# Kernel tuning notes

Hardware: AMD Instinct MI355X
Metric: run time of the kernel (lower is better)

Reference implementation:

```python
import jax, jax.numpy as jnp
import numpy as np

# ---- hardcoded module constants (from Cyborg.__init__) ----
B, S, V = 256, 128, 512
H = 30              # number of symbol vectors
N_STACKS = 2
R = 2               # REDUNDANCY
DEPTH = 4           # stack_depth
ZERO_OFFSET = 1e-6
NAND_BIAS = 3.0
INIT_SHARPEN = 10.0
N_VECS = 1 + N_STACKS  # input vec + one peek per stack = 3
C_BIG = (H + N_STACKS) * R   # 64 choices for push_fn / calc_out
C_SMALL = 2 * R              # 4 choices for pop_op / push_op


def _cossim(a, b, eps=1e-8):
    # torch.cosine_similarity semantics: per-vector norm clamp
    na = jnp.maximum(jnp.linalg.norm(a, axis=-1, keepdims=True), eps)
    nb = jnp.maximum(jnp.linalg.norm(b, axis=-1, keepdims=True), eps)
    return jnp.sum((a / na) * (b / nb), axis=-1)


def _nand(query, w, nw_raw):
    # Fuzzy-NAND gate bank (neurallambda NAND, clip='abs').
    # query: [B, N_VECS*V], w: [C, N_VECS*V], nw_raw: [C, N_VECS] -> [B, C]
    C = w.shape[0]
    q = query.reshape(-1, 1, N_VECS, V)
    wv = w.reshape(1, C, N_VECS, V)
    cos = jnp.abs(_cossim(q, wv))                 # [B, C, N_VECS], clip='abs'
    nw = jax.nn.sigmoid(nw_raw)[None]             # interpolate sim vs NOT(sim)
    interp = nw * cos + (1.0 - nw) * (1.0 - cos)
    return jnp.prod(interp, axis=-1)              # fuzzy AND over the 3 vecs


# ---- differentiable stack (soft pointer over DEPTH slots) ----
def _read(stack, ptr):
    return jnp.einsum('bdv,bd->bv', stack, ptr)

def _push(stack, ptr, val):
    p = jnp.roll(ptr, 1, axis=1)
    s = stack * (1.0 - p)[..., None] + val[:, None, :] * p[..., None]
    return s, p

def _pop(stack, ptr):
    s = stack * (1.0 - ptr)[..., None] + ZERO_OFFSET * ptr[..., None]
    p = jnp.roll(ptr, -1, axis=1)
    return s, p

def _pop_or_nop(stack, ptr, sharp, should_pop, should_nop):
    pr = jax.nn.softmax(jnp.stack([should_pop, should_nop], -1) * sharp, axis=-1)
    ps, pp = _pop(stack, ptr)
    s = ps * pr[:, 0, None, None] + stack * pr[:, 1, None, None]
    p = pp * pr[:, 0, None] + ptr * pr[:, 1, None]
    return s, p

def _push_or_nop(stack, ptr, sharp, should_push, should_nop, val):
    pr = jax.nn.softmax(jnp.stack([should_push, should_nop], -1) * sharp, axis=-1)
    ps, pp = _push(stack, ptr, val)
    s = ps * pr[:, 0, None, None] + stack * pr[:, 1, None, None]
    p = pp * pr[:, 0, None] + ptr * pr[:, 1, None]
    return s, p


def _forward(x, syms, stack_init_vec, sharp, pop_w, pop_nw, pushop_w, pushop_nw,
             pushfn_w, pushfn_nw, calc_w, calc_nw):
    b = x.shape[0]
    # init both stacks to zero_offset, pointer at slot 0, then hard-push init vec
    stack0 = jnp.full((N_STACKS, b, DEPTH, V), ZERO_OFFSET, x.dtype)
    ptr0 = jnp.zeros((N_STACKS, b, DEPTH), x.dtype).at[:, :, 0].set(1.0)
    init_val = jnp.broadcast_to(stack_init_vec, (b, V))
    stack0, ptr0 = jax.vmap(_push, in_axes=(0, 0, None))(stack0, ptr0, init_val)

    syms_b = jnp.broadcast_to(syms, (b, H, V))

    def step(carry, inp):
        stacks, ptrs = carry                                    # [2,B,D,V], [2,B,D]
        peeks = jax.vmap(_read)(stacks, ptrs)                   # [2,B,V]
        inps = jnp.concatenate([inp, peeks[0], peeks[1]], -1)   # [B,3V]
        out_opts = jnp.concatenate(
            [syms_b, peeks[0][:, None], peeks[1][:, None]], 1)  # [B,H+2,V]
        new_s, new_p = [], []
        for k in range(N_STACKS):
            pops = _nand(inps, pop_w[k], pop_nw[k])             # [B, 2R]
            pushes = _nand(inps, pushop_w[k], pushop_nw[k])     # [B, 2R]
            pv = _nand(inps, pushfn_w[k], pushfn_nw[k]).reshape(b, H + N_STACKS, R)
            push_val = jnp.einsum('bcv,bcr->bv', out_opts, pv)
            s, p = _pop_or_nop(stacks[k], ptrs[k], sharp[k],
                               pops[:, :R].max(1), pops[:, R:].max(1))
            s, p = _push_or_nop(s, p, sharp[k],
                                pushes[:, :R].max(1), pushes[:, R:].max(1), push_val)
            new_s.append(s)
            new_p.append(p)
        stacks = jnp.stack(new_s)
        ptrs = jnp.stack(new_p)
        peeks2 = jax.vmap(_read)(stacks, ptrs)
        inps2 = jnp.concatenate([inp, peeks2[0], peeks2[1]], -1)
        out_opts2 = jnp.concatenate(
            [syms_b, peeks2[0][:, None], peeks2[1][:, None]], 1)
        cv = _nand(inps2, calc_w, calc_nw).reshape(b, H + N_STACKS, R)
        out = jnp.einsum('bcv,bcr->bv', out_opts2, cv)
        return (stacks, ptrs), out

    _, outs = jax.lax.scan(step, (stack0, ptr0), jnp.swapaxes(x, 0, 1))
    return jnp.swapaxes(outs, 0, 1)  # [B,S,V]


def setup_inputs() -> dict:
    key = jax.random.key(0)
    ks = jax.random.split(key, 12)
    siv = jax.random.normal(ks[1], (V,), jnp.float32)
    siv = siv / jnp.linalg.norm(siv)
    return {
        'x': jax.random.normal(ks[0], (B, S, V), jnp.float32),
        'syms': jax.random.normal(ks[2], (H, V), jnp.float32),
        'stack_init_vec': siv,
        'sharp': jnp.full((N_STACKS,), INIT_SHARPEN, jnp.float32),
        'pop_w': jax.random.normal(ks[3], (N_STACKS, C_SMALL, N_VECS * V), jnp.float32),
        'pop_nw': jax.random.normal(ks[4], (N_STACKS, C_SMALL, N_VECS), jnp.float32) + NAND_BIAS,
        'pushop_w': jax.random.normal(ks[5], (N_STACKS, C_SMALL, N_VECS * V), jnp.float32),
        'pushop_nw': jax.random.normal(ks[6], (N_STACKS, C_SMALL, N_VECS), jnp.float32) + NAND_BIAS,
        'pushfn_w': jax.random.normal(ks[7], (N_STACKS, C_BIG, N_VECS * V), jnp.float32),
        'pushfn_nw': jax.random.normal(ks[8], (N_STACKS, C_BIG, N_VECS), jnp.float32) + NAND_BIAS,
        'calc_w': jax.random.normal(ks[9], (C_BIG, N_VECS * V), jnp.float32),
        'calc_nw': jax.random.normal(ks[10], (C_BIG, N_VECS), jnp.float32) + NAND_BIAS,
    }


def reference(x, syms, stack_init_vec, sharp, pop_w, pop_nw, pushop_w, pushop_nw,
              pushfn_w, pushfn_nw, calc_w, calc_nw):
    return _forward(x, syms, stack_init_vec, sharp, pop_w, pop_nw, pushop_w,
                    pushop_nw, pushfn_w, pushfn_nw, calc_w, calc_nw)
```

## Files before the change

### kernel.cpp

```cpp
#include <hip/hip_runtime.h>
#include <math.h>


#define SS 128
#define VV 512
#define NROWS 208
#define ZOFF 1e-6f

#define OFF_I0   0
#define OFF_OC   (32768*208)
#define OFF_GI   (OFF_OC + 32768*32)
#define OFF_M    (OFF_GI + 2*32*208)
#define OFF_A    (OFF_M + 1024)
#define OFF_Bc   (OFF_A + 624)
#define OFF_W0   (OFF_Bc + 624)

typedef _Float16 half8 __attribute__((ext_vector_type(8)));
typedef float f32x4 __attribute__((ext_vector_type(4)));
typedef float f32x2 __attribute__((ext_vector_type(2)));

__device__ __forceinline__ float rlane(float v, int lane) {
    return __int_as_float(__builtin_amdgcn_readlane(__float_as_int(v), lane));
}
template <int CTRL>
__device__ __forceinline__ float dpp_add(float x) {
    int y = __builtin_amdgcn_update_dpp(0, __float_as_int(x), CTRL, 0xF, 0xF, true);
    return x + __int_as_float(y);
}
__device__ __forceinline__ float sum16(float x) {
    x = dpp_add<0xB1>(x);
    x = dpp_add<0x4E>(x);
    x = dpp_add<0x124>(x);
    x = dpp_add<0x128>(x);
    return x;
}
__device__ __forceinline__ float swz16(float x) {
    return __int_as_float(__builtin_amdgcn_ds_swizzle(__float_as_int(x), 0x401F));
}

__device__ __forceinline__ const float* w_row(int r, const float* pw, const float* pow_,
                                              const float* pfw, const float* cw) {
    if (r < 8)   return pw   + r * 1536;
    if (r < 16)  return pow_ + (r - 8) * 1536;
    if (r < 144) return pfw  + (r - 16) * 1536;
    return cw + (r - 144) * 1536;
}
__device__ __forceinline__ const float* nw_row(int r, const float* pn, const float* pon,
                                               const float* pfn, const float* cn) {
    if (r < 8)   return pn   + r * 3;
    if (r < 16)  return pon  + (r - 8) * 3;
    if (r < 144) return pfn  + (r - 16) * 3;
    return cn + (r - 144) * 3;
}

__global__ void kB(const float* __restrict__ syms, const float* __restrict__ siv,
                   const float* __restrict__ pw, const float* __restrict__ pn,
                   const float* __restrict__ pow_, const float* __restrict__ pon,
                   const float* __restrict__ pfw, const float* __restrict__ pfn,
                   const float* __restrict__ cw, const float* __restrict__ cn,
                   float* __restrict__ ws) {
    int blk = blockIdx.x, tid = threadIdx.x;
    if (blk < 64) {
        int jj = blk >> 5, e = blk & 31;
        __shared__ float bas[512];
        for (int i = tid; i < 512; i += 256)
            bas[i] = (e == 0) ? 1.0f : ((e == 1) ? siv[i] : syms[(e - 2) * 512 + i]);
        __syncthreads();
        if (tid < NROWS) {
            int c = tid;
            const float4* w4 = (const float4*)(w_row(c, pw, pow_, pfw, cw) + (jj + 1) * 512);
            const float4* b4 = (const float4*)bas;
            float s = 0.f;
            for (int q = 0; q < 128; ++q) {
                float4 a = b4[q], b = w4[q];
                s += a.x * b.x + a.y * b.y + a.z * b.z + a.w * b.w;
            }
            ws[OFF_GI + (jj * 32 + e) * 208 + c] = s;
        }
    } else if (blk == 64) {
        __shared__ float basw[32 * 512];
        for (int i = tid; i < 32 * 512; i += 256) {
            int m = i >> 9, v = i & 511;
            basw[i] = (m == 0) ? 1.0f : ((m == 1) ? siv[v] : syms[(m - 2) * 512 + v]);
        }
        __syncthreads();
        for (int p = tid; p < 1024; p += 256) {
            int m = p >> 5, mm = p & 31;
            const float4* a4 = (const float4*)(basw + m * 512);
            const float4* b4 = (const float4*)(basw + mm * 512);
            float s = 0.f;
            for (int q = 0; q < 128; ++q) {
                float4 a = a4[q], b = b4[q];
                s += a.x * b.x + a.y * b.y + a.z * b.z + a.w * b.w;
            }
            ws[OFF_M + p] = s;
        }
    } else if (blk == 65) {
        for (int idx = tid; idx < 624; idx += 256) {
            int r = idx / 3, j = idx % 3;
            const float4* w4 = (const float4*)(w_row(r, pw, pow_, pfw, cw) + j * 512);
            float s = 0.f;
            for (int q = 0; q < 128; ++q) {
                float4 b = w4[q];
                s += b.x * b.x + b.y * b.y + b.z * b.z + b.w * b.w;
            }
            float nrm = fmaxf(sqrtf(s), 1e-8f);
            float nwv = nw_row(r, pn, pon, pfn, cn)[j];
            float sig = 1.f / (1.f + expf(-nwv));
            ws[OFF_A + idx]  = (2.f * sig - 1.f) / nrm;
            ws[OFF_Bc + idx] = 1.f - sig;
        }
    } else {
        int part = blk - 66;
        _Float16* whp = (_Float16*)(ws + OFF_W0);
        _Float16* wlp = whp + 208 * 512;
        for (int i = tid; i < 6656; i += 256) {
            int flat = part * 6656 + i;
            int c = flat >> 9, v = flat & 511;
            float wv = w_row(c, pw, pow_, pfw, cw)[v];
            _Float16 h = (_Float16)wv;
            whp[flat] = h;
            wlp[flat] = (_Float16)(wv - (float)h);
        }
    }
}

__global__ __launch_bounds__(256) void kA(const float* __restrict__ x, float* __restrict__ ws) {
    __shared__ half8 AH[2][256];
    __shared__ half8 AL[2][256];
    __shared__ float red[256];
    __shared__ float invx[64];
    const int tid = threadIdx.x;
    const int wid = tid >> 6, l = tid & 63;
    const int bid = blockIdx.x;
    const size_t bt0 = (size_t)(bid >> 1) * 64;

    const int sr = tid >> 2, ss = tid & 3;
    const float* xp = x + (bt0 + sr) * 512 + ss * 8;
    const int wpos = (sr >> 4) * 64 + (sr & 15) + (ss << 4);

    const _Float16* whp = (const _Float16*)(ws + OFF_W0);
    const _Float16* wlp = whp + 208 * 512;

    const int gw = ((bid & 1) << 2) | wid;
    const int nt = (gw < 5) ? 2 : 1;
    const int t0 = (gw < 5) ? (2 * gw) : (5 + gw);

    f32x4 acc[4][2];
#pragma unroll
    for (int m = 0; m < 4; ++m)
#pragma unroll
        for (int tt = 0; tt < 2; ++tt)
            acc[m][tt] = (f32x4){0.f, 0.f, 0.f, 0.f};

    float sumsq = 0.f;

    {
        float v[8];
        *(float4*)v       = *(const float4*)(xp);
        *(float4*)(v + 4) = *(const float4*)(xp + 4);
        half8 hh, hl;
#pragma unroll
        for (int j = 0; j < 8; ++j) {
            sumsq += v[j] * v[j];
            _Float16 h = (_Float16)v[j];
            hh[j] = h;
            hl[j] = (_Float16)(v[j] - (float)h);
        }
        AH[0][wpos] = hh;
        AL[0][wpos] = hl;
    }
    __syncthreads();

    for (int kt = 0; kt < 16; ++kt) {
        const int buf = kt & 1;
        half8 ahm[4], alm[4];
#pragma unroll
        for (int m = 0; m < 4; ++m) {
            ahm[m] = AH[buf][m * 64 + l];
            alm[m] = AL[buf][m * 64 + l];
        }
        float4 xv0, xv1;
        if (kt < 15) {
            xv0 = *(const float4*)(xp + (kt + 1) * 32);
            xv1 = *(const float4*)(xp + (kt + 1) * 32 + 4);
        }
        const int kof = kt * 32 + (l >> 4) * 8;
#pragma unroll
        for (int tt = 0; tt < 2; ++tt) {
            if (tt < nt) {
                const int c = (t0 + tt) * 16 + (l & 15);
                half8 bh = *(const half8*)(whp + c * 512 + kof);
                half8 bl = *(const half8*)(wlp + c * 512 + kof);
#pragma unroll
                for (int m = 0; m < 4; ++m) {
                    acc[m][tt] = __builtin_amdgcn_mfma_f32_16x16x32_f16(ahm[m], bh, acc[m][tt], 0, 0, 0);
                    acc[m][tt] = __builtin_amdgcn_mfma_f32_16x16x32_f16(ahm[m], bl, acc[m][tt], 0, 0, 0);
                    acc[m][tt] = __builtin_amdgcn_mfma_f32_16x16x32_f16(alm[m], bh, acc[m][tt], 0, 0, 0);
                }
            }
        }
        if (kt < 15) {
            float v[8];
            *(float4*)v = xv0; *(float4*)(v + 4) = xv1;
            half8 hh, hl;
#pragma unroll
            for (int j = 0; j < 8; ++j) {
                sumsq += v[j] * v[j];
                _Float16 h = (_Float16)v[j];
                hh[j] = h;
                hl[j] = (_Float16)(v[j] - (float)h);
            }
            AH[buf ^ 1][wpos] = hh;
            AL[buf ^ 1][wpos] = hl;
        }
        __syncthreads();
    }

    red[tid] = sumsq;
    __syncthreads();
    if (tid < 64) {
        float s = red[tid * 4] + red[tid * 4 + 1] + red[tid * 4 + 2] + red[tid * 4 + 3];
        invx[tid] = 1.f / fmaxf(sqrtf(s), 1e-8f);
    }
    __syncthreads();

#pragma unroll
    for (int tt = 0; tt < 2; ++tt) {
        if (tt < nt) {
            const int c = (t0 + tt) * 16 + (l & 15);
            const float A0 = ws[OFF_A + c * 3];
            const float B0 = ws[OFF_Bc + c * 3];
#pragma unroll
            for (int m = 0; m < 4; ++m) {
                const int rbase = m * 16 + (l >> 4) * 4;
#pragma unroll
                for (int j = 0; j < 4; ++j) {
                    const float ix = invx[rbase + j];
                    ws[OFF_I0 + (bt0 + rbase + j) * 208 + c] = A0 * fabsf(acc[m][tt][j]) * ix + B0;
                }
            }
        }
    }
}

__global__ __attribute__((amdgpu_flat_work_group_size(256, 256), amdgpu_waves_per_eu(1, 1)))
void kC(float* __restrict__ ws, const float* __restrict__ sharp,
        const float* __restrict__ syms, const float* __restrict__ siv,
        float* __restrict__ out) {
    __shared__ float nndL[2][144];
    __shared__ float ocL[2][32];
    const int b = blockIdx.x, tid = threadIdx.x;
    const int wid = tid >> 6, l = tid & 63;
    const int k = l >> 5, m = l & 31;
    const int isW3 = (wid == 3);
    const int isRow = (tid < 144);
    const int r = isW3 ? (144 + l) : tid;

    const float* GI = ws + OFF_GI;
    f32x2 GM1[32], GM2[32];
#pragma unroll
    for (int i = 0; i < 32; ++i) {
        float mv = ws[OFF_M + m * 32 + i];
        GM1[i] = (f32x2){GI[i * 208 + r], mv};
        GM2[i] = (f32x2){GI[(32 + i) * 208 + r], mv};
    }
    const float A1 = ws[OFF_A + r * 3 + 1],  A2 = ws[OFF_A + r * 3 + 2];
    const float B1 = ws[OFF_Bc + r * 3 + 1], B2 = ws[OFF_Bc + r * 3 + 2];
    const float sh = sharp[k];

    float2 sv2 = *(const float2*)(siv + 2 * tid);
    float2 sy[30];
#pragma unroll
    for (int mm = 0; mm < 30; ++mm)
        sy[mm] = *(const float2*)(syms + mm * 512 + 2 * tid);
    float* outb = out + (size_t)b * SS * 512 + 2 * tid;

    float st[4], p[4];
#pragma unroll
    for (int d = 0; d < 4; ++d) {
        st[d] = (d == 1) ? ((m == 1) ? 1.f : 0.f) : ((m == 0) ? ZOFF : 0.f);
        p[d] = (d == 1) ? 1.f : 0.f;
    }
    float pk = st[0] * p[0] + st[1] * p[1] + st[2] * p[2] + st[3] * p[3];
    float pkOther = __shfl_xor(pk, 32);

    const float* i0base = ws + OFF_I0 + (size_t)b * SS * 208;
    const int ioff = isW3 ? 0 : 1;
    float i0pro = i0base[r];
    float i0use = i0base[(size_t)ioff * 208 + r];

    auto CA = [&](float pp, float po, float iv) -> float {
        f32x2 a1 = (f32x2){0.f, 0.f}, b1 = (f32x2){0.f, 0.f};
        f32x2 a2 = (f32x2){0.f, 0.f}, b2 = (f32x2){0.f, 0.f};
#pragma unroll
        for (int mm = 0; mm < 32; ++mm) {
            float v0 = rlane(pp, mm);
            float v1 = rlane(pp, 32 + mm);
            if (mm & 1) { b1 += GM1[mm] * v0;  b2 += GM2[mm] * v1; }
            else        { a1 += GM1[mm] * v0;  a2 += GM2[mm] * v1; }
        }
        float dd1 = a1.x + b1.x, gq0 = a1.y + b1.y;
        float dd2 = a2.x + b2.x, gq1 = a2.y + b2.y;
        float pm0 = (k ? po : pp) * gq0;
        float pm1 = (k ? pp : po) * gq1;
        float q0 = sum16(pm0); q0 += swz16(q0);
        float q1 = sum16(pm1); q1 += swz16(q1);
        float iq0 = __frsqrt_rn(fmaxf(q0, 1e-16f));
        float iq1 = __frsqrt_rn(fmaxf(q1, 1e-16f));
        return iv * (A1 * fabsf(dd1) * iq0 + B1) * (A2 * fabsf(dd2) * iq1 + B2);
    };
    auto expand = [&](int buf, int t) {
        const float* ocp = ocL[buf];
        float4 c[8];
#pragma unroll
        for (int q = 0; q < 8; ++q) c[q] = *(const float4*)(ocp + 4 * q);
        float o0 = c[0].x + c[0].y * sv2.x;
        float o1 = c[0].x + c[0].y * sv2.y;
#pragma unroll
        for (int mm = 0; mm < 30; ++mm) {
            float cv = (mm + 2 < 4) ? ((mm + 2 == 2) ? c[0].z : c[0].w)
                                    : ((&c[0].x)[mm + 2]);
            o0 += cv * sy[mm].x;
            o1 += cv * sy[mm].y;
        }
        *(float2*)(outb + (size_t)t * 512) = (float2){o0, o1};
    };

    {
        float nv0 = CA(pk, pkOther, i0pro);
        if (isRow) nndL[0][tid] = nv0;
    }
    __syncthreads();

    for (int t = 0; t < SS; ++t) {
        int nidx = t + 1 + ioff; if (nidx > SS - 1) nidx = SS - 1;
        float i0nxt = i0base[(size_t)nidx * 208 + r];

        const float* nb = nndL[t & 1];
        float4 gp4 = *(const float4*)(nb + 4 * k);
        float4 gq4 = *(const float4*)(nb + 8 + 4 * k);
        float prp0 = 1.f / (1.f + __expf((fmaxf(gp4.z, gp4.w) - fmaxf(gp4.x, gp4.y)) * sh));
        float prq0 = 1.f / (1.f + __expf((fmaxf(gq4.z, gq4.w) - fmaxf(gq4.x, gq4.y)) * sh));
        float prp1 = 1.f - prp0, prq1 = 1.f - prq0;
        float prx = 0.f, pry = 0.f;
        if (m >= 2) {
            float2 pr2 = *(const float2*)(nb + 16 + 64 * k + 2 * m - 4);
            prx = pr2.x; pry = pr2.y;
        }
        float4 t30 = *(const float4*)(nb + 16 + 64 * k + 60);
        float pk0m = k ? pkOther : pk;
        float pk1m = k ? pk : pkOther;
        float pvc = prx + pry + (t30.x + t30.y) * pk0m + (t30.z + t30.w) * pk1m;

        float zc = (m == 0) ? ZOFF : 0.f;
        float s1v[4], p1[4];
#pragma unroll
        for (int d = 0; d < 4; ++d) {
            float ps = st[d] * (1.f - p[d]) + zc * p[d];
            s1v[d] = ps * prp0 + st[d] * prp1;
            p1[d] = p[(d + 1) & 3] * prp0 + p[d] * prp1;
        }
#pragma unroll
        for (int d = 0; d < 4; ++d) {
            float pu = p1[(d + 3) & 3];
            float su = s1v[d] * (1.f - pu) + pvc * pu;
            st[d] = su * prq0 + s1v[d] * prq1;
            p[d] = pu * prq0 + p1[d] * prq1;
        }
        float pkp = st[0] * p[0] + st[1] * p[1] + st[2] * p[2] + st[3] * p[3];
        float pkpOth = __shfl_xor(pkp, 32);

        if (t > 0) expand((t - 1) & 1, t - 1);

        float nv = CA(pkp, pkpOth, i0use);
        if (isRow) nndL[(t + 1) & 1][tid] = nv;
        if (isW3) {
            float s60 = rlane(nv, 60), s61 = rlane(nv, 61);
            float s62 = rlane(nv, 62), s63 = rlane(nv, 63);
            int src = (m >= 2) ? (2 * m - 4) : 0;
            float cx = __shfl(nv, src);
            float cy = __shfl(nv, src + 1);
            if (m < 2) { cx = 0.f; cy = 0.f; }
            if (l < 32) {
                float oc = cx + cy + (s60 + s61) * pkp + (s62 + s63) * pkpOth;
                ocL[t & 1][m] = oc;
            }
        }
        __syncthreads();
        pk = pkp;
        pkOther = pkpOth;
        i0use = i0nxt;
    }
    expand((SS - 1) & 1, SS - 1);
}

extern "C" void kernel_launch(void* const* d_in, const int* in_sizes, int n_in,
                              void* d_out, int out_size, void* d_ws, size_t ws_size,
                              hipStream_t stream) {
    const float* x    = (const float*)d_in[0];
    const float* syms = (const float*)d_in[1];
    const float* siv  = (const float*)d_in[2];
    const float* shp  = (const float*)d_in[3];
    const float* pw   = (const float*)d_in[4];
    const float* pn   = (const float*)d_in[5];
    const float* pow_ = (const float*)d_in[6];
    const float* pon  = (const float*)d_in[7];
    const float* pfw  = (const float*)d_in[8];
    const float* pfn  = (const float*)d_in[9];
    const float* cw   = (const float*)d_in[10];
    const float* cn   = (const float*)d_in[11];
    float* ws  = (float*)d_ws;
    float* out = (float*)d_out;

    hipLaunchKernelGGL(kB, dim3(82),   dim3(256), 0, stream,
                       syms, siv, pw, pn, pow_, pon, pfw, pfn, cw, cn, ws);
    hipLaunchKernelGGL(kA, dim3(1024), dim3(256), 0, stream, x, ws);
    hipLaunchKernelGGL(kC, dim3(256),  dim3(256), 0, stream, ws, shp, syms, siv, out);
}
```

Baseline: 358.6 us.

## Replicate gate rows per wave and compute gates via readlane to shorten serial step

Reassigns the 208 NAND rows across waves so each wave holds the 16 pop/push-op gate rows itself. The gate softmax probabilities are then computed in-register with readlane instead of being read back from shared memory after the barrier. Cross-half peek exchange now uses v_permlane32_swap instead of shfl. The output expansion is computed from a shared calc buffer with readlane broadcasts rather than through a separate oc staging step. The intent is to shorten the per-timestep critical path of the sequential recurrence, at the cost of redundant gate computation and more readlane traffic.

New measurement: 381.7 us. 1.06x slower.

```diff
diff --git a/kernel.cpp b/kernel.cpp
--- a/kernel.cpp
+++ b/kernel.cpp
@@ -36,6 +36,11 @@
 }
 __device__ __forceinline__ float swz16(float x) {
     return __int_as_float(__builtin_amdgcn_ds_swizzle(__float_as_int(x), 0x401F));
+}
+__device__ __forceinline__ void swap32(float x, float& lo, float& hi) {
+    float a = x, b = x;
+    asm("v_permlane32_swap_b32 %0, %1" : "+v"(a), "+v"(b));
+    lo = a; hi = b;
 }
 
 __device__ __forceinline__ const float* w_row(int r, const float* pw, const float* pow_,
@@ -154,7 +159,6 @@
             acc[m][tt] = (f32x4){0.f, 0.f, 0.f, 0.f};
 
     float sumsq = 0.f;
-
     {
         float v[8];
         *(float4*)v       = *(const float4*)(xp);
@@ -249,13 +253,18 @@
         const float* __restrict__ syms, const float* __restrict__ siv,
         float* __restrict__ out) {
     __shared__ float nndL[2][144];
-    __shared__ float ocL[2][32];
+    __shared__ float nnd2L[2][64];
     const int b = blockIdx.x, tid = threadIdx.x;
     const int wid = tid >> 6, l = tid & 63;
     const int k = l >> 5, m = l & 31;
-    const int isW3 = (wid == 3);
-    const int isRow = (tid < 144);
-    const int r = isW3 ? (144 + l) : tid;
+    int r;
+    if (l < 16)           r = l;
+    else if (wid == 0)    r = l;
+    else if (wid == 1)    r = 48 + l;
+    else if (wid == 2)    r = (l < 32) ? (176 + l) : (80 + l);
+    else                  r = 128 + l;
+    const bool isCalc = (r >= 144);
+    const bool wN = (r >= 16) && (r < 144);
 
     const float* GI = ws + OFF_GI;
     f32x2 GM1[32], GM2[32];
@@ -282,15 +291,18 @@
         st[d] = (d == 1) ? ((m == 1) ? 1.f : 0.f) : ((m == 0) ? ZOFF : 0.f);
         p[d] = (d == 1) ? 1.f : 0.f;
     }
-    float pk = st[0] * p[0] + st[1] * p[1] + st[2] * p[2] + st[3] * p[3];
-    float pkOther = __shfl_xor(pk, 32);
 
     const float* i0base = ws + OFF_I0 + (size_t)b * SS * 208;
-    const int ioff = isW3 ? 0 : 1;
-    float i0pro = i0base[r];
-    float i0use = i0base[(size_t)ioff * 208 + r];
-
-    auto CA = [&](float pp, float po, float iv) -> float {
+    const int ioff = isCalc ? 0 : 1;
+    float i0use;
+
+    float pk0c = 0.f, pk1c = 0.f;
+    float prpC = 0.f, prqC = 0.f;
+
+    auto CA = [&](float pp, float iv) -> float {
+        float lo, hi;
+        swap32(pp, lo, hi);
+        pk0c = lo; pk1c = hi;
         f32x2 a1 = (f32x2){0.f, 0.f}, b1 = (f32x2){0.f, 0.f};
         f32x2 a2 = (f32x2){0.f, 0.f}, b2 = (f32x2){0.f, 0.f};
 #pragma unroll
@@ -302,34 +314,32 @@
         }
         float dd1 = a1.x + b1.x, gq0 = a1.y + b1.y;
         float dd2 = a2.x + b2.x, gq1 = a2.y + b2.y;
-        float pm0 = (k ? po : pp) * gq0;
-        float pm1 = (k ? pp : po) * gq1;
+        float pm0 = pk0c * gq0;
+        float pm1 = pk1c * gq1;
         float q0 = sum16(pm0); q0 += swz16(q0);
         float q1 = sum16(pm1); q1 += swz16(q1);
         float iq0 = __frsqrt_rn(fmaxf(q0, 1e-16f));
         float iq1 = __frsqrt_rn(fmaxf(q1, 1e-16f));
         return iv * (A1 * fabsf(dd1) * iq0 + B1) * (A2 * fabsf(dd2) * iq1 + B2);
     };
-    auto expand = [&](int buf, int t) {
-        const float* ocp = ocL[buf];
-        float4 c[8];
-#pragma unroll
-        for (int q = 0; q < 8; ++q) c[q] = *(const float4*)(ocp + 4 * q);
-        float o0 = c[0].x + c[0].y * sv2.x;
-        float o1 = c[0].x + c[0].y * sv2.y;
-#pragma unroll
-        for (int mm = 0; mm < 30; ++mm) {
-            float cv = (mm + 2 < 4) ? ((mm + 2 == 2) ? c[0].z : c[0].w)
-                                    : ((&c[0].x)[mm + 2]);
-            o0 += cv * sy[mm].x;
-            o1 += cv * sy[mm].y;
-        }
-        *(float2*)(outb + (size_t)t * 512) = (float2){o0, o1};
+    auto gates = [&](float nv) {
+        float g[16];
+#pragma unroll
+        for (int i = 0; i < 16; ++i) g[i] = rlane(nv, i);
+        float dp = k ? (fmaxf(g[6],  g[7])  - fmaxf(g[4],  g[5]))
+                     : (fmaxf(g[2],  g[3])  - fmaxf(g[0],  g[1]));
+        float dq = k ? (fmaxf(g[14], g[15]) - fmaxf(g[12], g[13]))
+                     : (fmaxf(g[10], g[11]) - fmaxf(g[8],  g[9]));
+        prpC = 1.f / (1.f + __expf(dp * sh));
+        prqC = 1.f / (1.f + __expf(dq * sh));
     };
 
     {
-        float nv0 = CA(pk, pkOther, i0pro);
-        if (isRow) nndL[0][tid] = nv0;
+        float pk = st[0] * p[0] + st[1] * p[1] + st[2] * p[2] + st[3] * p[3];
+        float nv0 = CA(pk, i0base[r]);
+        if (wN) nndL[0][r] = nv0;
+        gates(nv0);
+        i0use = i0base[(size_t)ioff * 208 + r];
     }
     __syncthreads();
 
@@ -337,22 +347,38 @@
         int nidx = t + 1 + ioff; if (nidx > SS - 1) nidx = SS - 1;
         float i0nxt = i0base[(size_t)nidx * 208 + r];
 
+        if (t > 0) {
+            const float* n2 = nnd2L[(t - 1) & 1];
+            float cx = 0.f, cy = 0.f;
+            if (m >= 2) {
+                float2 c2 = *(const float2*)(n2 + 2 * m - 4);
+                cx = c2.x; cy = c2.y;
+            }
+            float4 c30 = *(const float4*)(n2 + 60);
+            float ocv = cx + cy + (c30.x + c30.y) * pk0c + (c30.z + c30.w) * pk1c;
+            float oc0 = rlane(ocv, 0), oc1 = rlane(ocv, 1);
+            float o0 = oc0 + oc1 * sv2.x;
+            float o1 = oc0 + oc1 * sv2.y;
+#pragma unroll
+            for (int mm = 0; mm < 30; ++mm) {
+                float cv = rlane(ocv, 2 + mm);
+                o0 += cv * sy[mm].x;
+                o1 += cv * sy[mm].y;
+            }
+            *(float2*)(outb + (size_t)(t - 1) * 512) = make_float2(o0, o1);
+        }
+
         const float* nb = nndL[t & 1];
-        float4 gp4 = *(const float4*)(nb + 4 * k);
-        float4 gq4 = *(const float4*)(nb + 8 + 4 * k);
-        float prp0 = 1.f / (1.f + __expf((fmaxf(gp4.z, gp4.w) - fmaxf(gp4.x, gp4.y)) * sh));
-        float prq0 = 1.f / (1.f + __expf((fmaxf(gq4.z, gq4.w) - fmaxf(gq4.x, gq4.y)) * sh));
-        float prp1 = 1.f - prp0, prq1 = 1.f - prq0;
         float prx = 0.f, pry = 0.f;
         if (m >= 2) {
             float2 pr2 = *(const float2*)(nb + 16 + 64 * k + 2 * m - 4);
             prx = pr2.x; pry = pr2.y;
         }
         float4 t30 = *(const float4*)(nb + 16 + 64 * k + 60);
-        float pk0m = k ? pkOther : pk;
-        float pk1m = k ? pk : pkOther;
-        float pvc = prx + pry + (t30.x + t30.y) * pk0m + (t30.z + t30.w) * pk1m;
-
+        float pvc = prx + pry + (t30.x + t30.y) * pk0c + (t30.z + t30.w) * pk1c;
+
+        float prp0 = prpC, prq0 = prqC;
+        float prp1 = 1.f - prp0, prq1 = 1.f - prq0;
         float zc = (m == 0) ? ZOFF : 0.f;
         float s1v[4], p1[4];
 #pragma unroll
@@ -369,30 +395,35 @@
             p[d] = pu * prq0 + p1[d] * prq1;
         }
         float pkp = st[0] * p[0] + st[1] * p[1] + st[2] * p[2] + st[3] * p[3];
-        float pkpOth = __shfl_xor(pkp, 32);
-
-        if (t > 0) expand((t - 1) & 1, t - 1);
-
-        float nv = CA(pkp, pkpOth, i0use);
-        if (isRow) nndL[(t + 1) & 1][tid] = nv;
-        if (isW3) {
-            float s60 = rlane(nv, 60), s61 = rlane(nv, 61);
-            float s62 = rlane(nv, 62), s63 = rlane(nv, 63);
-            int src = (m >= 2) ? (2 * m - 4) : 0;
-            float cx = __shfl(nv, src);
-            float cy = __shfl(nv, src + 1);
-            if (m < 2) { cx = 0.f; cy = 0.f; }
-            if (l < 32) {
-                float oc = cx + cy + (s60 + s61) * pkp + (s62 + s63) * pkpOth;
-                ocL[t & 1][m] = oc;
-            }
-        }
+
+        float nv = CA(pkp, i0use);
+        if (wN) nndL[(t + 1) & 1][r] = nv;
+        if (isCalc) nnd2L[t & 1][r - 144] = nv;
+        gates(nv);
         __syncthreads();
-        pk = pkp;
-        pkOther = pkpOth;
         i0use = i0nxt;
     }
-    expand((SS - 1) & 1, SS - 1);
+
+    {
+        const float* n2 = nnd2L[(SS - 1) & 1];
+        float cx = 0.f, cy = 0.f;
+        if (m >= 2) {
+            float2 c2 = *(const float2*)(n2 + 2 * m - 4);
+            cx = c2.x; cy = c2.y;
+        }
+        float4 c30 = *(const float4*)(n2 + 60);
+        float ocv = cx + cy + (c30.x + c30.y) * pk0c + (c30.z + c30.w) * pk1c;
+        float oc0 = rlane(ocv, 0), oc1 = rlane(ocv, 1);
+        float o0 = oc0 + oc1 * sv2.x;
+        float o1 = oc0 + oc1 * sv2.y;
+#pragma unroll
+        for (int mm = 0; mm < 30; ++mm) {
+            float cv = rlane(ocv, 2 + mm);
+            o0 += cv * sy[mm].x;
+            o1 += cv * sy[mm].y;
+        }
+        *(float2*)(outb + (size_t)(SS - 1) * 512) = make_float2(o0, o1);
+    }
 }
 
 extern "C" void kernel_launch(void* const* d_in, const int* in_sizes, int n_in,
```

## Defer output expansion out of the serial recurrence into a batched epilogue

Applied to the files above, without the earlier changes.

Each step's output coefficients are now kept in a shared-memory array covering all 128 timesteps, and the per-step expansion against the symbol vectors is removed from the serial loop. After the loop, all threads expand the stored coefficients into outputs using float4 loads and stores. This shortens the latency-bound sequential loop and frees registers that held symbol data during it. The cost is a separate, non-overlapped epilogue, extra shared memory, and higher register use in the epilogue.

After: 371.4 us. 1.04x slower.

```diff
diff --git a/kernel.cpp b/kernel.cpp
--- a/kernel.cpp
+++ b/kernel.cpp
@@ -154,7 +154,6 @@
             acc[m][tt] = (f32x4){0.f, 0.f, 0.f, 0.f};
 
     float sumsq = 0.f;
-
     {
         float v[8];
         *(float4*)v       = *(const float4*)(xp);
@@ -249,7 +248,7 @@
         const float* __restrict__ syms, const float* __restrict__ siv,
         float* __restrict__ out) {
     __shared__ float nndL[2][144];
-    __shared__ float ocL[2][32];
+    __shared__ float ocA[SS * 36];
     const int b = blockIdx.x, tid = threadIdx.x;
     const int wid = tid >> 6, l = tid & 63;
     const int k = l >> 5, m = l & 31;
@@ -268,13 +267,6 @@
     const float A1 = ws[OFF_A + r * 3 + 1],  A2 = ws[OFF_A + r * 3 + 2];
     const float B1 = ws[OFF_Bc + r * 3 + 1], B2 = ws[OFF_Bc + r * 3 + 2];
     const float sh = sharp[k];
-
-    float2 sv2 = *(const float2*)(siv + 2 * tid);
-    float2 sy[30];
-#pragma unroll
-    for (int mm = 0; mm < 30; ++mm)
-        sy[mm] = *(const float2*)(syms + mm * 512 + 2 * tid);
-    float* outb = out + (size_t)b * SS * 512 + 2 * tid;
 
     float st[4], p[4];
 #pragma unroll
@@ -310,22 +302,6 @@
         float iq1 = __frsqrt_rn(fmaxf(q1, 1e-16f));
         return iv * (A1 * fabsf(dd1) * iq0 + B1) * (A2 * fabsf(dd2) * iq1 + B2);
     };
-    auto expand = [&](int buf, int t) {
-        const float* ocp = ocL[buf];
-        float4 c[8];
-#pragma unroll
-        for (int q = 0; q < 8; ++q) c[q] = *(const float4*)(ocp + 4 * q);
-        float o0 = c[0].x + c[0].y * sv2.x;
-        float o1 = c[0].x + c[0].y * sv2.y;
-#pragma unroll
-        for (int mm = 0; mm < 30; ++mm) {
-            float cv = (mm + 2 < 4) ? ((mm + 2 == 2) ? c[0].z : c[0].w)
-                                    : ((&c[0].x)[mm + 2]);
-            o0 += cv * sy[mm].x;
-            o1 += cv * sy[mm].y;
-        }
-        *(float2*)(outb + (size_t)t * 512) = (float2){o0, o1};
-    };
 
     {
         float nv0 = CA(pk, pkOther, i0pro);
@@ -370,8 +346,6 @@
         }
         float pkp = st[0] * p[0] + st[1] * p[1] + st[2] * p[2] + st[3] * p[3];
         float pkpOth = __shfl_xor(pkp, 32);
-
-        if (t > 0) expand((t - 1) & 1, t - 1);
 
         float nv = CA(pkp, pkpOth, i0use);
         if (isRow) nndL[(t + 1) & 1][tid] = nv;
@@ -384,7 +358,7 @@
             if (m < 2) { cx = 0.f; cy = 0.f; }
             if (l < 32) {
                 float oc = cx + cy + (s60 + s61) * pkp + (s62 + s63) * pkpOth;
-                ocL[t & 1][m] = oc;
+                ocA[t * 36 + m] = oc;
             }
         }
         __syncthreads();
@@ -392,7 +366,39 @@
         pkOther = pkpOth;
         i0use = i0nxt;
     }
-    expand((SS - 1) & 1, SS - 1);
+    __syncthreads();
+
+    {
+        const int vc = (tid & 127) * 4;
+        const int te0 = (tid >> 7) * 64;
+        float4 sv4 = *(const float4*)(siv + vc);
+        float4 sy4[30];
+#pragma unroll
+        for (int mm = 0; mm < 30; ++mm)
+            sy4[mm] = *(const float4*)(syms + mm * 512 + vc);
+        float* outb = out + (size_t)b * SS * 512 + vc;
+        for (int tt = 0; tt < 64; ++tt) {
+            const int t = te0 + tt;
+            const float* ocp = ocA + t * 36;
+            float4 c[8];
+#pragma unroll
+            for (int q = 0; q < 8; ++q) c[q] = *(const float4*)(ocp + 4 * q);
+            const float* cf = &c[0].x;
+            float o0 = cf[0] + cf[1] * sv4.x;
+            float o1 = cf[0] + cf[1] * sv4.y;
+            float o2 = cf[0] + cf[1] * sv4.z;
+            float o3 = cf[0] + cf[1] * sv4.w;
+#pragma unroll
+            for (int mm = 0; mm < 30; ++mm) {
+                float cv = cf[2 + mm];
+                o0 += cv * sy4[mm].x;
+                o1 += cv * sy4[mm].y;
+                o2 += cv * sy4[mm].z;
+                o3 += cv * sy4[mm].w;
+            }
+            *(float4*)(outb + (size_t)t * 512) = make_float4(o0, o1, o2, o3);
+        }
+    }
 }
 
 extern "C" void kernel_launch(void* const* d_in, const int* in_sizes, int n_in,
```
